# Kernel tuning notes

Hardware: AMD Instinct MI355X
Metric: run time of the kernel (lower is better)

## Reference

```python
import jax, jax.numpy as jnp
import numpy as np

N = 1_000_000
D = 256          # in_features == hidden_features (required by norm_out)
B = 4096         # number of graphs/segments
TEMP = 0.4
LN_EPS = 1e-5


def _layernorm(h, w, b):
    mu = jnp.mean(h, axis=-1, keepdims=True)
    var = jnp.mean(jnp.square(h - mu), axis=-1, keepdims=True)
    return (h - mu) * jax.lax.rsqrt(var + LN_EPS) * w + b


def setup_inputs() -> dict:
    key = jax.random.key(0)
    ks = jax.random.split(key, 8)
    x = jax.random.normal(ks[0], (N, D), dtype=jnp.float32)
    batch = jnp.sort(jax.random.randint(ks[1], (N,), 0, B)).astype(jnp.int32)
    W1 = jax.random.normal(ks[2], (D, D), dtype=jnp.float32) * 0.02
    b1 = jnp.zeros((D,), dtype=jnp.float32)
    ln1_w = jnp.ones((D,), dtype=jnp.float32)
    ln1_b = jnp.zeros((D,), dtype=jnp.float32)
    W2 = jax.random.normal(ks[3], (1, D), dtype=jnp.float32) * 0.02
    ln2_w = jnp.ones((D,), dtype=jnp.float32)
    ln2_b = jnp.zeros((D,), dtype=jnp.float32)
    return {"x": x, "batch": batch, "W1": W1, "b1": b1, "ln1_w": ln1_w,
            "ln1_b": ln1_b, "W2": W2, "ln2_w": ln2_w, "ln2_b": ln2_b}


def reference(x, batch, W1, b1, ln1_w, ln1_b, W2, ln2_w, ln2_b):
    # project: Linear -> LayerNorm -> GELU -> Linear(1, no bias)
    h = x @ W1.T + b1                               # [N, D]
    h = jax.nn.gelu(_layernorm(h, ln1_w, ln1_b), approximate=False)
    w = h @ W2.T                                    # [N, 1] attention logits
    # segment softmax with temperature (subtract max BEFORE dividing by T,
    # exactly as in the original module)
    w_max = jax.ops.segment_max(w, batch, num_segments=B)     # [B, 1]
    w = jnp.exp((w - w_max[batch]) / TEMP)                    # [N, 1]
    w_sum = jax.ops.segment_sum(w, batch, num_segments=B)    # [B, 1]
    w = w / (w_sum[batch] + 1e-6)                             # [N, 1]
    out = jax.ops.segment_sum(x * w, batch, num_segments=B)  # [B, D]
    return _layernorm(out, ln2_w, ln2_b)
```

## Files before the change

kernel.cpp:

```cpp
#include <hip/hip_runtime.h>
#include <cstdint>

#define D 256
#define TEMP_INV 2.5f
#define LN_EPS 1e-5f

using short8  = __attribute__((ext_vector_type(8))) short;
using floatx4 = __attribute__((ext_vector_type(4))) float;

__device__ __forceinline__ unsigned short f2bf(float f) {
    unsigned u = __builtin_bit_cast(unsigned, f);
    u += 0x7fffu + ((u >> 16) & 1u);
    return (unsigned short)(u >> 16);
}

__device__ __forceinline__ int gran_off(int rt, int m, int kt, int q) {
    int swz = (kt * 2 + (q & 1)) & 15;
    return (kt * 4 + rt) * 64 + q * 16 + (m ^ swz);
}

__global__ void k_conv_w1(const float* __restrict__ w1, unsigned short* __restrict__ w1b) {
    int i = (blockIdx.x * 256 + threadIdx.x) * 4;
    float4 v = *(const float4*)(w1 + i);
    ushort4 o;
    o.x = f2bf(v.x); o.y = f2bf(v.y); o.z = f2bf(v.z); o.w = f2bf(v.w);
    *(ushort4*)(w1b + i) = o;
}

__global__ void k_seg_bounds(const int* __restrict__ batch, int* __restrict__ seg,
                             int N, int B) {
    int t = blockIdx.x * 256 + threadIdx.x;
    if (t > B) return;
    int lo = 0, hi = N;
    while (lo < hi) { int mid = (lo + hi) >> 1; if (batch[mid] < t) lo = mid + 1; else hi = mid; }
    seg[t] = lo;
}

__global__ __launch_bounds__(256) void k_logits(
    const float* __restrict__ x, const unsigned short* __restrict__ w1b,
    const float* __restrict__ b1, const float* __restrict__ ln1w,
    const float* __restrict__ ln1b, const float* __restrict__ w2,
    float* __restrict__ logits)
{
    __shared__ uint4 ldsX[2048];
    __shared__ float redS[64], redQ[64], redL[64];

    const int t = threadIdx.x;
    const int row0 = blockIdx.x * 64;

    {
        const float4* xf4 = (const float4*)x;
        #pragma unroll
        for (int it = 0; it < 8; ++it) {
            int c = it * 256 + t;
            int row = c >> 5, j = c & 31;
            long base = (long)(row0 + row) * 64 + j * 2;
            float4 a = xf4[base], b = xf4[base + 1];
            union { uint4 u; unsigned short s[8]; } g;
            g.s[0] = f2bf(a.x); g.s[1] = f2bf(a.y); g.s[2] = f2bf(a.z); g.s[3] = f2bf(a.w);
            g.s[4] = f2bf(b.x); g.s[5] = f2bf(b.y); g.s[6] = f2bf(b.z); g.s[7] = f2bf(b.w);
            ldsX[gran_off(row >> 4, row & 15, j >> 2, j & 3)] = g.u;
        }
    }
    __syncthreads();

    const int wave = t >> 6, lane = t & 63;
    const int q = lane >> 4, m = lane & 15;

    floatx4 acc[4][4];
    #pragma unroll
    for (int a = 0; a < 4; ++a)
        #pragma unroll
        for (int b = 0; b < 4; ++b)
            acc[a][b] = (floatx4){0.f, 0.f, 0.f, 0.f};

    const uint4* w1b4 = (const uint4*)w1b;
    #pragma unroll
    for (int kt = 0; kt < 8; ++kt) {
        uint4 afu[4];
        #pragma unroll
        for (int rt = 0; rt < 4; ++rt) afu[rt] = ldsX[gran_off(rt, m, kt, q)];
        #pragma unroll
        for (int ct = 0; ct < 4; ++ct) {
            int col = wave * 64 + ct * 16 + m;
            uint4 bfu = w1b4[col * 32 + kt * 4 + q];
            short8 bfr = __builtin_bit_cast(short8, bfu);
            #pragma unroll
            for (int rt = 0; rt < 4; ++rt)
                acc[rt][ct] = __builtin_amdgcn_mfma_f32_16x16x32_bf16(
                    __builtin_bit_cast(short8, afu[rt]), bfr, acc[rt][ct], 0, 0, 0);
        }
    }

    __syncthreads();
    if (t < 64) { redS[t] = 0.f; redQ[t] = 0.f; redL[t] = 0.f; }
    __syncthreads();

    float b1c[4], lwc[4], lbc[4], w2c[4];
    #pragma unroll
    for (int ct = 0; ct < 4; ++ct) {
        int col = wave * 64 + ct * 16 + m;
        b1c[ct] = b1[col]; lwc[ct] = ln1w[col]; lbc[ct] = ln1b[col]; w2c[ct] = w2[col];
    }

    float ps[4][4], pq[4][4];
    #pragma unroll
    for (int rt = 0; rt < 4; ++rt) {
        #pragma unroll
        for (int reg = 0; reg < 4; ++reg) {
            float s = 0.f, ss = 0.f;
            #pragma unroll
            for (int ct = 0; ct < 4; ++ct) {
                float v = acc[rt][ct][reg] + b1c[ct];
                acc[rt][ct][reg] = v;
                s += v; ss += v * v;
            }
            #pragma unroll
            for (int off = 1; off < 16; off <<= 1) {
                s  += __shfl_xor(s, off);
                ss += __shfl_xor(ss, off);
            }
            ps[rt][reg] = s; pq[rt][reg] = ss;
        }
    }
    if (m == 0) {
        #pragma unroll
        for (int rt = 0; rt < 4; ++rt)
            #pragma unroll
            for (int reg = 0; reg < 4; ++reg) {
                atomicAdd(&redS[rt * 16 + q * 4 + reg], ps[rt][reg]);
                atomicAdd(&redQ[rt * 16 + q * 4 + reg], pq[rt][reg]);
            }
    }
    __syncthreads();

    float pl[4][4];
    #pragma unroll
    for (int rt = 0; rt < 4; ++rt) {
        #pragma unroll
        for (int reg = 0; reg < 4; ++reg) {
            int r = rt * 16 + q * 4 + reg;
            float mu  = redS[r] * (1.f / 256.f);
            float var = redQ[r] * (1.f / 256.f) - mu * mu;
            float rstd = rsqrtf(var + LN_EPS);
            float s = 0.f;
            #pragma unroll
            for (int ct = 0; ct < 4; ++ct) {
                float v = (acc[rt][ct][reg] - mu) * rstd * lwc[ct] + lbc[ct];
                float g = 0.5f * v * (1.f + erff(v * 0.70710678f));
                s += g * w2c[ct];
            }
            #pragma unroll
            for (int off = 1; off < 16; off <<= 1) s += __shfl_xor(s, off);
            pl[rt][reg] = s;
        }
    }
    if (m == 0) {
        #pragma unroll
        for (int rt = 0; rt < 4; ++rt)
            #pragma unroll
            for (int reg = 0; reg < 4; ++reg)
                atomicAdd(&redL[rt * 16 + q * 4 + reg], pl[rt][reg]);
    }
    __syncthreads();
    if (t < 64) logits[row0 + t] = redL[t];
}

__global__ __launch_bounds__(64) void k_segstats(float* __restrict__ w,
                                                 const int* __restrict__ seg) {
    int b = blockIdx.x, lane = threadIdx.x;
    int s = seg[b], e = seg[b + 1], n = e - s;
    if (n <= 0) return;
    float mx = -3.4e38f;
    for (int i = lane; i < n; i += 64) mx = fmaxf(mx, w[s + i]);
    #pragma unroll
    for (int off = 1; off < 64; off <<= 1) mx = fmaxf(mx, __shfl_xor(mx, off));
    float sum = 0.f;
    for (int i = lane; i < n; i += 64) sum += __expf((w[s + i] - mx) * TEMP_INV);
    #pragma unroll
    for (int off = 1; off < 64; off <<= 1) sum += __shfl_xor(sum, off);
    float inv = 1.f / (sum + 1e-6f);
    for (int i = lane; i < n; i += 64) w[s + i] = __expf((w[s + i] - mx) * TEMP_INV) * inv;
}

__global__ __launch_bounds__(256) void k_pool(
    const float* __restrict__ x, const float* __restrict__ coef,
    const int* __restrict__ seg, const float* __restrict__ ln2w,
    const float* __restrict__ ln2b, float* __restrict__ out)
{
    int b = blockIdx.x, t = threadIdx.x;
    int s = seg[b], e = seg[b + 1], n = e - s;
    const float* xp = x + (long)s * D + t;
    const float* cp = coef + s;
    float acc = 0.f;
    int i = 0;
    for (; i + 4 <= n; i += 4) {
        float c0 = cp[i], c1 = cp[i + 1], c2 = cp[i + 2], c3 = cp[i + 3];
        float v0 = xp[(long)i * D], v1 = xp[(long)(i + 1) * D];
        float v2 = xp[(long)(i + 2) * D], v3 = xp[(long)(i + 3) * D];
        acc += c0 * v0; acc += c1 * v1; acc += c2 * v2; acc += c3 * v3;
    }
    for (; i < n; ++i) acc += cp[i] * xp[(long)i * D];

    __shared__ float rb[8];
    float v = acc, vv = acc * acc;
    #pragma unroll
    for (int off = 1; off < 64; off <<= 1) { v += __shfl_xor(v, off); vv += __shfl_xor(vv, off); }
    int wid = t >> 6, lane = t & 63;
    if (lane == 0) { rb[wid] = v; rb[4 + wid] = vv; }
    __syncthreads();
    float sum = rb[0] + rb[1] + rb[2] + rb[3];
    float sq  = rb[4] + rb[5] + rb[6] + rb[7];
    float mu  = sum * (1.f / (float)D);
    float var = sq * (1.f / (float)D) - mu * mu;
    float rstd = rsqrtf(var + LN_EPS);
    out[(long)b * D + t] = (acc - mu) * rstd * ln2w[t] + ln2b[t];
}

extern "C" void kernel_launch(void* const* d_in, const int* in_sizes, int n_in,
                              void* d_out, int out_size, void* d_ws, size_t ws_size,
                              hipStream_t stream) {
    const float* x    = (const float*)d_in[0];
    const int*   batch= (const int*)d_in[1];
    const float* W1   = (const float*)d_in[2];
    const float* b1   = (const float*)d_in[3];
    const float* ln1w = (const float*)d_in[4];
    const float* ln1b = (const float*)d_in[5];
    const float* W2   = (const float*)d_in[6];
    const float* ln2w = (const float*)d_in[7];
    const float* ln2b = (const float*)d_in[8];
    float* out = (float*)d_out;

    int N = in_sizes[0] / D;
    int B = out_size / D;

    char* ws = (char*)d_ws;
    unsigned short* w1b = (unsigned short*)ws;
    float* wcoef = (float*)(ws + 131072);
    size_t segoff = 131072 + (((size_t)N * 4 + 127) & ~(size_t)127);
    int* seg = (int*)(ws + segoff);

    k_conv_w1   <<<(D * D) / 1024, 256, 0, stream>>>(W1, w1b);
    k_seg_bounds<<<(B + 256) / 256, 256, 0, stream>>>(batch, seg, N, B);
    k_logits    <<<N / 64, 256, 0, stream>>>(x, w1b, b1, ln1w, ln1b, W2, wcoef);
    k_segstats  <<<B, 64, 0, stream>>>(wcoef, seg);
    k_pool      <<<B, 256, 0, stream>>>(x, wcoef, seg, ln2w, ln2b, out);
}
```

Before: 1.973 ms.

## Replace LDS atomics with per-wave partials, fast GELU, vectorized pooling, occupancy hint

In the logits kernel, shared-memory atomics and the zero-init barrier are replaced by per-wave partial arrays that are summed after one barrier. The epilogue parameter loads are hoisted ahead of the MFMA loop. erff is replaced by an Abramowitz-Stegun polynomial approximation, and a min-blocks launch bound of 4 is added. Segment softmax now stores the exponentials and rescales them instead of recomputing exp. Pooling now has each wave take rows with float4 loads and sums the per-wave partials in LDS, which trades some GELU accuracy and register headroom for less memory traffic.

```diff
diff --git a/kernel.cpp b/kernel.cpp
--- a/kernel.cpp
+++ b/kernel.cpp
@@ -12,6 +12,21 @@
     unsigned u = __builtin_bit_cast(unsigned, f);
     u += 0x7fffu + ((u >> 16) & 1u);
     return (unsigned short)(u >> 16);
+}
+
+__device__ __forceinline__ float gelu_f(float v) {
+    float x  = v * 0.70710678118f;
+    float ax = fabsf(x);
+    float t  = __builtin_amdgcn_rcpf(fmaf(0.3275911f, ax, 1.f));
+    float p  = fmaf(1.061405429f, t, -1.453152027f);
+    p = fmaf(p, t, 1.421413741f);
+    p = fmaf(p, t, -0.284496736f);
+    p = fmaf(p, t, 0.254829592f);
+    p = p * t;
+    float e  = __expf(-x * x);
+    float er = fmaf(-p, e, 1.f);
+    er = copysignf(er, x);
+    return 0.5f * v * (1.f + er);
 }
 
 __device__ __forceinline__ int gran_off(int rt, int m, int kt, int q) {
@@ -36,14 +51,14 @@
     seg[t] = lo;
 }
 
-__global__ __launch_bounds__(256) void k_logits(
+__global__ __launch_bounds__(256, 4) void k_logits(
     const float* __restrict__ x, const unsigned short* __restrict__ w1b,
     const float* __restrict__ b1, const float* __restrict__ ln1w,
     const float* __restrict__ ln1b, const float* __restrict__ w2,
     float* __restrict__ logits)
 {
     __shared__ uint4 ldsX[2048];
-    __shared__ float redS[64], redQ[64], redL[64];
+    __shared__ float redS[256], redQ[256], redL[256];
 
     const int t = threadIdx.x;
     const int row0 = blockIdx.x * 64;
@@ -67,6 +82,13 @@
     const int wave = t >> 6, lane = t & 63;
     const int q = lane >> 4, m = lane & 15;
 
+    float b1c[4], lwc[4], lbc[4], w2c[4];
+    #pragma unroll
+    for (int ct = 0; ct < 4; ++ct) {
+        int col = wave * 64 + ct * 16 + m;
+        b1c[ct] = b1[col]; lwc[ct] = ln1w[col]; lbc[ct] = ln1b[col]; w2c[ct] = w2[col];
+    }
+
     floatx4 acc[4][4];
     #pragma unroll
     for (int a = 0; a < 4; ++a)
@@ -92,18 +114,6 @@
         }
     }
 
-    __syncthreads();
-    if (t < 64) { redS[t] = 0.f; redQ[t] = 0.f; redL[t] = 0.f; }
-    __syncthreads();
-
-    float b1c[4], lwc[4], lbc[4], w2c[4];
-    #pragma unroll
-    for (int ct = 0; ct < 4; ++ct) {
-        int col = wave * 64 + ct * 16 + m;
-        b1c[ct] = b1[col]; lwc[ct] = ln1w[col]; lbc[ct] = ln1b[col]; w2c[ct] = w2[col];
-    }
-
-    float ps[4][4], pq[4][4];
     #pragma unroll
     for (int rt = 0; rt < 4; ++rt) {
         #pragma unroll
@@ -120,50 +130,38 @@
                 s  += __shfl_xor(s, off);
                 ss += __shfl_xor(ss, off);
             }
-            ps[rt][reg] = s; pq[rt][reg] = ss;
-        }
-    }
-    if (m == 0) {
-        #pragma unroll
-        for (int rt = 0; rt < 4; ++rt)
-            #pragma unroll
-            for (int reg = 0; reg < 4; ++reg) {
-                atomicAdd(&redS[rt * 16 + q * 4 + reg], ps[rt][reg]);
-                atomicAdd(&redQ[rt * 16 + q * 4 + reg], pq[rt][reg]);
-            }
-    }
-    __syncthreads();
-
-    float pl[4][4];
+            if (m == 0) {
+                int r = rt * 16 + q * 4 + reg;
+                redS[wave * 64 + r] = s;
+                redQ[wave * 64 + r] = ss;
+            }
+        }
+    }
+    __syncthreads();
+
     #pragma unroll
     for (int rt = 0; rt < 4; ++rt) {
         #pragma unroll
         for (int reg = 0; reg < 4; ++reg) {
             int r = rt * 16 + q * 4 + reg;
-            float mu  = redS[r] * (1.f / 256.f);
-            float var = redQ[r] * (1.f / 256.f) - mu * mu;
+            float sum = redS[r] + redS[64 + r] + redS[128 + r] + redS[192 + r];
+            float sq  = redQ[r] + redQ[64 + r] + redQ[128 + r] + redQ[192 + r];
+            float mu  = sum * (1.f / 256.f);
+            float var = sq * (1.f / 256.f) - mu * mu;
             float rstd = rsqrtf(var + LN_EPS);
             float s = 0.f;
             #pragma unroll
             for (int ct = 0; ct < 4; ++ct) {
                 float v = (acc[rt][ct][reg] - mu) * rstd * lwc[ct] + lbc[ct];
-                float g = 0.5f * v * (1.f + erff(v * 0.70710678f));
-                s += g * w2c[ct];
+                s += gelu_f(v) * w2c[ct];
             }
             #pragma unroll
             for (int off = 1; off < 16; off <<= 1) s += __shfl_xor(s, off);
-            pl[rt][reg] = s;
-        }
-    }
-    if (m == 0) {
-        #pragma unroll
-        for (int rt = 0; rt < 4; ++rt)
-            #pragma unroll
-            for (int reg = 0; reg < 4; ++reg)
-                atomicAdd(&redL[rt * 16 + q * 4 + reg], pl[rt][reg]);
-    }
-    __syncthreads();
-    if (t < 64) logits[row0 + t] = redL[t];
+            if (m == 0) redL[wave * 64 + r] = s;
+        }
+    }
+    __syncthreads();
+    if (t < 64) logits[row0 + t] = redL[t] + redL[64 + t] + redL[128 + t] + redL[192 + t];
 }
 
 __global__ __launch_bounds__(64) void k_segstats(float* __restrict__ w,
@@ -176,11 +174,15 @@
     #pragma unroll
     for (int off = 1; off < 64; off <<= 1) mx = fmaxf(mx, __shfl_xor(mx, off));
     float sum = 0.f;
-    for (int i = lane; i < n; i += 64) sum += __expf((w[s + i] - mx) * TEMP_INV);
+    for (int i = lane; i < n; i += 64) {
+        float p = __expf((w[s + i] - mx) * TEMP_INV);
+        sum += p;
+        w[s + i] = p;
+    }
     #pragma unroll
     for (int off = 1; off < 64; off <<= 1) sum += __shfl_xor(sum, off);
     float inv = 1.f / (sum + 1e-6f);
-    for (int i = lane; i < n; i += 64) w[s + i] = __expf((w[s + i] - mx) * TEMP_INV) * inv;
+    for (int i = lane; i < n; i += 64) w[s + i] *= inv;
 }
 
 __global__ __launch_bounds__(256) void k_pool(
@@ -189,25 +191,43 @@
     const float* __restrict__ ln2b, float* __restrict__ out)
 {
     int b = blockIdx.x, t = threadIdx.x;
+    int wave = t >> 6, lane = t & 63;
     int s = seg[b], e = seg[b + 1], n = e - s;
-    const float* xp = x + (long)s * D + t;
+
+    const float4* xp = (const float4*)x + (long)s * 64 + lane;
     const float* cp = coef + s;
-    float acc = 0.f;
-    int i = 0;
-    for (; i + 4 <= n; i += 4) {
-        float c0 = cp[i], c1 = cp[i + 1], c2 = cp[i + 2], c3 = cp[i + 3];
-        float v0 = xp[(long)i * D], v1 = xp[(long)(i + 1) * D];
-        float v2 = xp[(long)(i + 2) * D], v3 = xp[(long)(i + 3) * D];
-        acc += c0 * v0; acc += c1 * v1; acc += c2 * v2; acc += c3 * v3;
-    }
-    for (; i < n; ++i) acc += cp[i] * xp[(long)i * D];
+
+    float4 a0 = {0.f, 0.f, 0.f, 0.f}, a1 = {0.f, 0.f, 0.f, 0.f};
+    int i = wave;
+    for (; i + 4 < n; i += 8) {
+        float c0 = cp[i], c1 = cp[i + 4];
+        float4 v0 = xp[(long)i * 64];
+        float4 v1 = xp[(long)(i + 4) * 64];
+        a0.x = fmaf(c0, v0.x, a0.x); a0.y = fmaf(c0, v0.y, a0.y);
+        a0.z = fmaf(c0, v0.z, a0.z); a0.w = fmaf(c0, v0.w, a0.w);
+        a1.x = fmaf(c1, v1.x, a1.x); a1.y = fmaf(c1, v1.y, a1.y);
+        a1.z = fmaf(c1, v1.z, a1.z); a1.w = fmaf(c1, v1.w, a1.w);
+    }
+    for (; i < n; i += 4) {
+        float c = cp[i];
+        float4 v = xp[(long)i * 64];
+        a0.x = fmaf(c, v.x, a0.x); a0.y = fmaf(c, v.y, a0.y);
+        a0.z = fmaf(c, v.z, a0.z); a0.w = fmaf(c, v.w, a0.w);
+    }
+    float4 acc4;
+    acc4.x = a0.x + a1.x; acc4.y = a0.y + a1.y;
+    acc4.z = a0.z + a1.z; acc4.w = a0.w + a1.w;
+
+    __shared__ float part[4][256];
+    *(float4*)&part[wave][lane * 4] = acc4;
+    __syncthreads();
+    float acc = part[0][t] + part[1][t] + part[2][t] + part[3][t];
 
     __shared__ float rb[8];
     float v = acc, vv = acc * acc;
     #pragma unroll
     for (int off = 1; off < 64; off <<= 1) { v += __shfl_xor(v, off); vv += __shfl_xor(vv, off); }
-    int wid = t >> 6, lane = t & 63;
-    if (lane == 0) { rb[wid] = v; rb[4 + wid] = vv; }
+    if (lane == 0) { rb[wave] = v; rb[4 + wave] = vv; }
     __syncthreads();
     float sum = rb[0] + rb[1] + rb[2] + rb[3];
     float sq  = rb[4] + rb[5] + rb[6] + rb[7];
```

After: 1.691 ms. -14.3%, faster.
